# Optimization experiments

Measured on AMD Instinct MI355X. Metric: run time of the kernel, lower is better.

The kernel has to match this reference:

```python
import jax, jax.numpy as jnp
import numpy as np

LAMDA = 1.0


def setup_inputs() -> dict:
    key = jax.random.key(0)
    k1, k2, k3, k4 = jax.random.split(key, 4)
    B, C, D = 16384, 1000, 512
    logits = jax.random.normal(k1, (B, C), dtype=jnp.float32)
    labels = jax.random.randint(k2, (B,), 0, C, dtype=jnp.int64)
    features = jax.random.normal(k3, (B, D), dtype=jnp.float32)
    global_protos = jax.random.normal(k4, (C, D), dtype=jnp.float32)
    return {"logits": logits, "labels": labels, "features": features,
            "global_protos": global_protos}


def reference(logits, labels, features, global_protos):
    # --- classification loss: mean cross-entropy ---
    logp = jax.nn.log_softmax(logits, axis=-1)                 # [B, C]
    ce_loss = -jnp.take_along_axis(logp, labels[:, None], axis=1).mean()
    ce_loss = jnp.where(jnp.isfinite(ce_loss), ce_loss, 0.0)

    # --- prototype alignment loss ---
    # Every label has a (finite) global prototype, so the per-sample dict
    # loop reduces to: gather proto by label, per-sample MSE, mean over B.
    gathered = global_protos[labels]                           # [B, D]
    per_sample_mse = jnp.mean((features - gathered) ** 2, axis=-1)  # [B]
    proto_loss = per_sample_mse.mean()

    total_loss = ce_loss + LAMDA * proto_loss
    total_loss = jnp.where(jnp.isfinite(total_loss), total_loss, ce_loss)
    return (total_loss, ce_loss, proto_loss)
```

## Files before the change

### kernel.cpp

```cpp
#include <hip/hip_runtime.h>
#include <math.h>


#ifndef INFINITY
#define INFINITY __builtin_inff()
#endif

__global__ __launch_bounds__(256) void fedtgp_rows(
    const float* __restrict__ logits,
    const int*   __restrict__ labels,
    const float* __restrict__ features,
    const float* __restrict__ protos,
    double2* __restrict__ part,
    int B, int C, int D)
{
    const int tid  = threadIdx.x;
    const int lane = tid & 63;
    const int wv   = tid >> 6;
    const int row  = blockIdx.x * 4 + wv;
    const bool valid = (row < B);

    double2 res;
    res.x = 0.0; res.y = 0.0;

    if (valid) {
        const int    lab  = labels[row];
        const float* lrow = logits + (size_t)row * C;
        const float4* l4  = (const float4*)lrow;
        const int C4 = C >> 2;
        const int D4 = D >> 2;

        float4 v[4];
        #pragma unroll
        for (int k = 0; k < 4; ++k) {
            const int idx = lane + 64 * k;
            v[k] = (idx < C4) ? l4[idx]
                              : make_float4(-INFINITY, -INFINITY, -INFINITY, -INFINITY);
        }
        const float4* f4 = (const float4*)(features + (size_t)row * D);
        const float4* p4 = (const float4*)(protos   + (size_t)lab * D);
        float4 f0 = make_float4(0.f,0.f,0.f,0.f), p0 = f0, f1 = f0, p1 = f0;
        if (lane < D4)      { f0 = f4[lane];      p0 = p4[lane]; }
        if (lane + 64 < D4) { f1 = f4[lane + 64]; p1 = p4[lane + 64]; }
        const float ll = lrow[lab];

        float s = 0.f;
        #pragma unroll
        for (int k = 0; k < 4; ++k) {
            s += __expf(v[k].x) + __expf(v[k].y)
               + __expf(v[k].z) + __expf(v[k].w);
        }
        for (int idx = 256 + lane; idx < C4; idx += 64) {
            const float4 w = l4[idx];
            s += __expf(w.x) + __expf(w.y) + __expf(w.z) + __expf(w.w);
        }
        for (int c = (C4 << 2) + lane; c < C; c += 64)
            s += __expf(lrow[c]);

        float q;
        {
            const float ax = f0.x - p0.x, ay = f0.y - p0.y;
            const float az = f0.z - p0.z, aw = f0.w - p0.w;
            const float bx = f1.x - p1.x, by = f1.y - p1.y;
            const float bz = f1.z - p1.z, bw = f1.w - p1.w;
            q = ax*ax + ay*ay + az*az + aw*aw
              + bx*bx + by*by + bz*bz + bw*bw;
        }
        for (int idx = lane + 128; idx < D4; idx += 64) {
            const float4 f = f4[idx];
            const float4 p = p4[idx];
            const float dx = f.x - p.x, dy = f.y - p.y;
            const float dz = f.z - p.z, dw = f.w - p.w;
            q += dx*dx + dy*dy + dz*dz + dw*dw;
        }
        for (int d = (D4 << 2) + lane; d < D; d += 64)
        {
            const float df = features[(size_t)row * D + d]
                           - protos[(size_t)lab * D + d];
            q += df * df;
        }

        #pragma unroll
        for (int off = 32; off > 0; off >>= 1) {
            s += __shfl_xor(s, off, 64);
            q += __shfl_xor(q, off, 64);
        }

        res.x = (double)(__logf(s) - ll);
        res.y = (double)(q / (float)D);
    }

    if (lane == 0)
        part[blockIdx.x * 4 + wv] = res;
}

__global__ __launch_bounds__(1024) void fedtgp_finalize(
    const double2* __restrict__ part,
    float* __restrict__ out,
    int npart, double invB)
{
    const int tid  = threadIdx.x;
    const int lane = tid & 63;
    const int wv   = tid >> 6;
    __shared__ double rc[16];
    __shared__ double rp[16];

    double c = 0.0, p = 0.0;
    for (int i = tid; i < npart; i += 1024) {
        const double2 v = part[i];
        c += v.x;
        p += v.y;
    }
    #pragma unroll
    for (int off = 32; off > 0; off >>= 1) {
        c += __shfl_xor(c, off, 64);
        p += __shfl_xor(p, off, 64);
    }
    if (lane == 0) { rc[wv] = c; rp[wv] = p; }
    __syncthreads();

    if (tid == 0) {
        double cs = 0.0, ps = 0.0;
        #pragma unroll
        for (int k = 0; k < 16; ++k) { cs += rc[k]; ps += rp[k]; }
        float ce = (float)(cs * invB);
        float pl = (float)(ps * invB);
        if (!isfinite(ce)) ce = 0.0f;
        float tot = ce + pl;
        if (!isfinite(tot)) tot = ce;
        out[0] = tot;
        out[1] = ce;
        out[2] = pl;
    }
}

extern "C" void kernel_launch(void* const* d_in, const int* in_sizes, int n_in,
                              void* d_out, int out_size, void* d_ws, size_t ws_size,
                              hipStream_t stream)
{
    const float* logits   = (const float*)d_in[0];
    const int*   labels   = (const int*)  d_in[1];
    const float* features = (const float*)d_in[2];
    const float* protos   = (const float*)d_in[3];
    float* out = (float*)d_out;

    const int B = in_sizes[1];
    const int C = in_sizes[0] / B;
    const int D = in_sizes[2] / B;

    int nb = (B + 3) / 4;
    const size_t need = (size_t)nb * 4 * sizeof(double2);
    if (need > ws_size) {
        nb = (int)(ws_size / (4 * sizeof(double2)));
        if (nb < 1) nb = 1;
    }
    const int npart = nb * 4;

    double2* part = (double2*)d_ws;

    fedtgp_rows<<<nb, 256, 0, stream>>>(logits, labels, features, protos,
                                        part, B, C, D);
    fedtgp_finalize<<<1, 1024, 0, stream>>>(part, out, npart, 1.0 / (double)B);
}
```

Measured before the change: 125.8 us.

## Fuse finalize into row kernel via last-block atomic reduction and nontemporal loads

Merges the separate finalize kernel into the main row kernel. Each block reduces its four rows in shared memory, writes one partial pair with atomics, and the last block to increment a counter sums all partials and writes the outputs. Logits and features are read with nontemporal loads to reduce cache pollution. This removes a kernel launch and shrinks the partial array, but adds a memset of the counter header, atomics and a threadfence in every block.

```diff
diff --git a/kernel.cpp b/kernel.cpp
--- a/kernel.cpp
+++ b/kernel.cpp
@@ -6,13 +6,26 @@
 #define INFINITY __builtin_inff()
 #endif
 
-__global__ __launch_bounds__(256) void fedtgp_rows(
+typedef float fx4 __attribute__((ext_vector_type(4)));
+
+struct Header {
+    unsigned int cnt;
+    unsigned int pad[15];
+};
+
+__device__ __forceinline__ fx4 nt_load4(const float* p) {
+    return __builtin_nontemporal_load((const fx4*)p);
+}
+
+__global__ __launch_bounds__(256) void fedtgp_fused2(
     const float* __restrict__ logits,
     const int*   __restrict__ labels,
     const float* __restrict__ features,
     const float* __restrict__ protos,
-    double2* __restrict__ part,
-    int B, int C, int D)
+    Header* __restrict__ hdr,
+    unsigned long long* __restrict__ part,
+    float* __restrict__ out,
+    int B, int C, int D, double invB)
 {
     const int tid  = threadIdx.x;
     const int lane = tid & 63;
@@ -20,28 +33,30 @@
     const int row  = blockIdx.x * 4 + wv;
     const bool valid = (row < B);
 
-    double2 res;
-    res.x = 0.0; res.y = 0.0;
+    __shared__ double sc[4], sp[4];
+
+    double ce_w = 0.0, pl_w = 0.0;
 
     if (valid) {
         const int    lab  = labels[row];
         const float* lrow = logits + (size_t)row * C;
-        const float4* l4  = (const float4*)lrow;
         const int C4 = C >> 2;
         const int D4 = D >> 2;
 
-        float4 v[4];
+        fx4 v[4];
         #pragma unroll
         for (int k = 0; k < 4; ++k) {
             const int idx = lane + 64 * k;
-            v[k] = (idx < C4) ? l4[idx]
-                              : make_float4(-INFINITY, -INFINITY, -INFINITY, -INFINITY);
+            if (idx < C4) v[k] = nt_load4(lrow + 4 * idx);
+            else          v[k] = (fx4){-INFINITY, -INFINITY, -INFINITY, -INFINITY};
         }
-        const float4* f4 = (const float4*)(features + (size_t)row * D);
-        const float4* p4 = (const float4*)(protos   + (size_t)lab * D);
-        float4 f0 = make_float4(0.f,0.f,0.f,0.f), p0 = f0, f1 = f0, p1 = f0;
-        if (lane < D4)      { f0 = f4[lane];      p0 = p4[lane]; }
-        if (lane + 64 < D4) { f1 = f4[lane + 64]; p1 = p4[lane + 64]; }
+        const float* frow = features + (size_t)row * D;
+        const float* prow = protos   + (size_t)lab * D;
+        fx4 f0 = (fx4){0.f,0.f,0.f,0.f}, p0 = f0, f1 = f0, p1 = f0;
+        if (lane < D4)      { f0 = nt_load4(frow + 4 * lane);
+                              p0 = *(const fx4*)(prow + 4 * lane); }
+        if (lane + 64 < D4) { f1 = nt_load4(frow + 4 * (lane + 64));
+                              p1 = *(const fx4*)(prow + 4 * (lane + 64)); }
         const float ll = lrow[lab];
 
         float s = 0.f;
@@ -51,7 +66,7 @@
                + __expf(v[k].z) + __expf(v[k].w);
         }
         for (int idx = 256 + lane; idx < C4; idx += 64) {
-            const float4 w = l4[idx];
+            const fx4 w = *(const fx4*)(lrow + 4 * idx);
             s += __expf(w.x) + __expf(w.y) + __expf(w.z) + __expf(w.w);
         }
         for (int c = (C4 << 2) + lane; c < C; c += 64)
@@ -67,16 +82,14 @@
               + bx*bx + by*by + bz*bz + bw*bw;
         }
         for (int idx = lane + 128; idx < D4; idx += 64) {
-            const float4 f = f4[idx];
-            const float4 p = p4[idx];
+            const fx4 f = *(const fx4*)(frow + 4 * idx);
+            const fx4 p = *(const fx4*)(prow + 4 * idx);
             const float dx = f.x - p.x, dy = f.y - p.y;
             const float dz = f.z - p.z, dw = f.w - p.w;
             q += dx*dx + dy*dy + dz*dz + dw*dw;
         }
-        for (int d = (D4 << 2) + lane; d < D; d += 64)
-        {
-            const float df = features[(size_t)row * D + d]
-                           - protos[(size_t)lab * D + d];
+        for (int d = (D4 << 2) + lane; d < D; d += 64) {
+            const float df = frow[d] - prow[d];
             q += df * df;
         }
 
@@ -86,51 +99,58 @@
             q += __shfl_xor(q, off, 64);
         }
 
-        res.x = (double)(__logf(s) - ll);
-        res.y = (double)(q / (float)D);
+        ce_w = (double)(__logf(s) - ll);
+        pl_w = (double)(q / (float)D);
     }
 
-    if (lane == 0)
-        part[blockIdx.x * 4 + wv] = res;
-}
-
-__global__ __launch_bounds__(1024) void fedtgp_finalize(
-    const double2* __restrict__ part,
-    float* __restrict__ out,
-    int npart, double invB)
-{
-    const int tid  = threadIdx.x;
-    const int lane = tid & 63;
-    const int wv   = tid >> 6;
-    __shared__ double rc[16];
-    __shared__ double rp[16];
-
-    double c = 0.0, p = 0.0;
-    for (int i = tid; i < npart; i += 1024) {
-        const double2 v = part[i];
-        c += v.x;
-        p += v.y;
-    }
-    #pragma unroll
-    for (int off = 32; off > 0; off >>= 1) {
-        c += __shfl_xor(c, off, 64);
-        p += __shfl_xor(p, off, 64);
-    }
-    if (lane == 0) { rc[wv] = c; rp[wv] = p; }
+    if (lane == 0) { sc[wv] = ce_w; sp[wv] = pl_w; }
     __syncthreads();
 
     if (tid == 0) {
-        double cs = 0.0, ps = 0.0;
+        const double ce_b = sc[0] + sc[1] + sc[2] + sc[3];
+        const double pl_b = sp[0] + sp[1] + sp[2] + sp[3];
+        atomicExch(&part[(size_t)blockIdx.x * 2 + 0], __double_as_longlong(ce_b));
+        atomicExch(&part[(size_t)blockIdx.x * 2 + 1], __double_as_longlong(pl_b));
+        __threadfence();
+    }
+    __syncthreads();
+
+    __shared__ bool amLast;
+    if (tid == 0) {
+        const unsigned prev = atomicAdd(&hdr->cnt, 1u);
+        amLast = (prev == (unsigned)(gridDim.x - 1));
+    }
+    __syncthreads();
+
+    if (amLast) {
+        const int n2 = (int)gridDim.x;
+        double c = 0.0, p = 0.0;
+        for (int i = tid; i < n2; i += 256) {
+            const unsigned long long cb = atomicAdd(&part[(size_t)i * 2 + 0], 0ull);
+            const unsigned long long pb = atomicAdd(&part[(size_t)i * 2 + 1], 0ull);
+            c += __longlong_as_double(cb);
+            p += __longlong_as_double(pb);
+        }
         #pragma unroll
-        for (int k = 0; k < 16; ++k) { cs += rc[k]; ps += rp[k]; }
-        float ce = (float)(cs * invB);
-        float pl = (float)(ps * invB);
-        if (!isfinite(ce)) ce = 0.0f;
-        float tot = ce + pl;
-        if (!isfinite(tot)) tot = ce;
-        out[0] = tot;
-        out[1] = ce;
-        out[2] = pl;
+        for (int off = 32; off > 0; off >>= 1) {
+            c += __shfl_xor(c, off, 64);
+            p += __shfl_xor(p, off, 64);
+        }
+        __shared__ double rc[4], rp[4];
+        if (lane == 0) { rc[wv] = c; rp[wv] = p; }
+        __syncthreads();
+        if (tid == 0) {
+            const double cs = rc[0] + rc[1] + rc[2] + rc[3];
+            const double ps = rp[0] + rp[1] + rp[2] + rp[3];
+            float ce = (float)(cs * invB);
+            float pl = (float)(ps * invB);
+            if (!isfinite(ce)) ce = 0.0f;
+            float tot = ce + pl;
+            if (!isfinite(tot)) tot = ce;
+            out[0] = tot;
+            out[1] = ce;
+            out[2] = pl;
+        }
     }
 }
 
@@ -149,16 +169,18 @@
     const int D = in_sizes[2] / B;
 
     int nb = (B + 3) / 4;
-    const size_t need = (size_t)nb * 4 * sizeof(double2);
+    const size_t need = sizeof(Header) + (size_t)nb * 2 * sizeof(unsigned long long);
     if (need > ws_size) {
-        nb = (int)(ws_size / (4 * sizeof(double2)));
+        nb = (int)((ws_size - sizeof(Header)) / (2 * sizeof(unsigned long long)));
         if (nb < 1) nb = 1;
     }
-    const int npart = nb * 4;
 
-    double2* part = (double2*)d_ws;
+    Header* hdr = (Header*)d_ws;
+    unsigned long long* part = (unsigned long long*)((char*)d_ws + sizeof(Header));
 
-    fedtgp_rows<<<nb, 256, 0, stream>>>(logits, labels, features, protos,
-                                        part, B, C, D);
-    fedtgp_finalize<<<1, 1024, 0, stream>>>(part, out, npart, 1.0 / (double)B);
+    (void)hipMemsetAsync(d_ws, 0, sizeof(Header), stream);
+
+    fedtgp_fused2<<<nb, 256, 0, stream>>>(logits, labels, features, protos,
+                                          hdr, part, out, B, C, D,
+                                          1.0 / (double)B);
 }
```

New measurement: 309.9 us. 146% more time.

## Process four rows per wave with double-buffered prefetch and nontemporal loads

Applied to the files above, without the earlier changes.

Each wave now handles four consecutive rows instead of one, issuing the loads for the next row before reducing the current one so memory latency overlaps with the exp and MSE work. Logits and features are read with nontemporal loads to avoid polluting cache, while prototypes still use normal loads because rows are reused across samples. The grid shrinks by a factor of four, giving fewer waves in flight and more registers per thread, which can cut the parallelism available to hide latency.

```diff
diff --git a/kernel.cpp b/kernel.cpp
--- a/kernel.cpp
+++ b/kernel.cpp
@@ -5,6 +5,31 @@
 #ifndef INFINITY
 #define INFINITY __builtin_inff()
 #endif
+
+typedef float fx4 __attribute__((ext_vector_type(4)));
+
+__device__ __forceinline__ fx4 nt_load4(const float* p) {
+    return __builtin_nontemporal_load((const fx4*)p);
+}
+
+__device__ __forceinline__ void load_row(
+    const float* __restrict__ lrow, const float* __restrict__ frow,
+    const float* __restrict__ prow, int lane, int C4, int D4, int lab,
+    fx4 v[4], fx4& f0, fx4& f1, fx4& p0, fx4& p1, float& ll)
+{
+    #pragma unroll
+    for (int k = 0; k < 4; ++k) {
+        const int idx = lane + 64 * k;
+        if (idx < C4) v[k] = nt_load4(lrow + 4 * idx);
+        else          v[k] = (fx4){-INFINITY, -INFINITY, -INFINITY, -INFINITY};
+    }
+    f0 = p0 = f1 = p1 = (fx4){0.f, 0.f, 0.f, 0.f};
+    if (lane < D4)      { f0 = nt_load4(frow + 4 * lane);
+                          p0 = *(const fx4*)(prow + 4 * lane); }
+    if (lane + 64 < D4) { f1 = nt_load4(frow + 4 * (lane + 64));
+                          p1 = *(const fx4*)(prow + 4 * (lane + 64)); }
+    ll = lrow[lab];
+}
 
 __global__ __launch_bounds__(256) void fedtgp_rows(
     const float* __restrict__ logits,
@@ -17,81 +42,104 @@
     const int tid  = threadIdx.x;
     const int lane = tid & 63;
     const int wv   = tid >> 6;
-    const int row  = blockIdx.x * 4 + wv;
-    const bool valid = (row < B);
-
-    double2 res;
-    res.x = 0.0; res.y = 0.0;
-
-    if (valid) {
-        const int    lab  = labels[row];
-        const float* lrow = logits + (size_t)row * C;
-        const float4* l4  = (const float4*)lrow;
-        const int C4 = C >> 2;
-        const int D4 = D >> 2;
-
-        float4 v[4];
-        #pragma unroll
-        for (int k = 0; k < 4; ++k) {
-            const int idx = lane + 64 * k;
-            v[k] = (idx < C4) ? l4[idx]
-                              : make_float4(-INFINITY, -INFINITY, -INFINITY, -INFINITY);
+    const int wave = blockIdx.x * 4 + wv;
+    const int base_row = wave * 4;
+
+    const int C4 = C >> 2;
+    const int D4 = D >> 2;
+
+    fx4 v[2][4], f0[2], f1[2], p0[2], p1[2];
+    float ll[2];
+    const float* lrow[2];
+    const float* frow[2];
+    const float* prow[2];
+    bool ok[2];
+
+    double ce_acc = 0.0, pl_acc = 0.0;
+
+    {
+        const int row = base_row;
+        ok[0] = (row < B);
+        if (ok[0]) {
+            const int lab = labels[row];
+            lrow[0] = logits   + (size_t)row * C;
+            frow[0] = features + (size_t)row * D;
+            prow[0] = protos   + (size_t)lab * D;
+            load_row(lrow[0], frow[0], prow[0], lane, C4, D4, lab,
+                     v[0], f0[0], f1[0], p0[0], p1[0], ll[0]);
         }
-        const float4* f4 = (const float4*)(features + (size_t)row * D);
-        const float4* p4 = (const float4*)(protos   + (size_t)lab * D);
-        float4 f0 = make_float4(0.f,0.f,0.f,0.f), p0 = f0, f1 = f0, p1 = f0;
-        if (lane < D4)      { f0 = f4[lane];      p0 = p4[lane]; }
-        if (lane + 64 < D4) { f1 = f4[lane + 64]; p1 = p4[lane + 64]; }
-        const float ll = lrow[lab];
-
-        float s = 0.f;
-        #pragma unroll
-        for (int k = 0; k < 4; ++k) {
-            s += __expf(v[k].x) + __expf(v[k].y)
-               + __expf(v[k].z) + __expf(v[k].w);
+    }
+
+    #pragma unroll
+    for (int r = 0; r < 4; ++r) {
+        const int cur = r & 1;
+        const int nxt = cur ^ 1;
+
+        if (r + 1 < 4) {
+            const int row = base_row + r + 1;
+            ok[nxt] = (row < B);
+            if (ok[nxt]) {
+                const int lab = labels[row];
+                lrow[nxt] = logits   + (size_t)row * C;
+                frow[nxt] = features + (size_t)row * D;
+                prow[nxt] = protos   + (size_t)lab * D;
+                load_row(lrow[nxt], frow[nxt], prow[nxt], lane, C4, D4, lab,
+                         v[nxt], f0[nxt], f1[nxt], p0[nxt], p1[nxt], ll[nxt]);
+            }
         }
-        for (int idx = 256 + lane; idx < C4; idx += 64) {
-            const float4 w = l4[idx];
-            s += __expf(w.x) + __expf(w.y) + __expf(w.z) + __expf(w.w);
+
+        if (ok[cur]) {
+            float s = 0.f;
+            #pragma unroll
+            for (int k = 0; k < 4; ++k) {
+                s += __expf(v[cur][k].x) + __expf(v[cur][k].y)
+                   + __expf(v[cur][k].z) + __expf(v[cur][k].w);
+            }
+            for (int idx = 256 + lane; idx < C4; idx += 64) {
+                const fx4 w = *(const fx4*)(lrow[cur] + 4 * idx);
+                s += __expf(w.x) + __expf(w.y) + __expf(w.z) + __expf(w.w);
+            }
+            for (int c = (C4 << 2) + lane; c < C; c += 64)
+                s += __expf(lrow[cur][c]);
+
+            float q;
+            {
+                const float ax = f0[cur].x - p0[cur].x, ay = f0[cur].y - p0[cur].y;
+                const float az = f0[cur].z - p0[cur].z, aw = f0[cur].w - p0[cur].w;
+                const float bx = f1[cur].x - p1[cur].x, by = f1[cur].y - p1[cur].y;
+                const float bz = f1[cur].z - p1[cur].z, bw = f1[cur].w - p1[cur].w;
+                q = ax*ax + ay*ay + az*az + aw*aw
+                  + bx*bx + by*by + bz*bz + bw*bw;
+            }
+            for (int idx = lane + 128; idx < D4; idx += 64) {
+                const fx4 f = *(const fx4*)(frow[cur] + 4 * idx);
+                const fx4 p = *(const fx4*)(prow[cur] + 4 * idx);
+                const float dx = f.x - p.x, dy = f.y - p.y;
+                const float dz = f.z - p.z, dw = f.w - p.w;
+                q += dx*dx + dy*dy + dz*dz + dw*dw;
+            }
+            for (int d = (D4 << 2) + lane; d < D; d += 64) {
+                const float df = frow[cur][d] - prow[cur][d];
+                q += df * df;
+            }
+
+            #pragma unroll
+            for (int off = 32; off > 0; off >>= 1) {
+                s += __shfl_xor(s, off, 64);
+                q += __shfl_xor(q, off, 64);
+            }
+
+            if (lane == 0) {
+                ce_acc += (double)(__logf(s) - ll[cur]);
+                pl_acc += (double)(q / (float)D);
+            }
         }
-        for (int c = (C4 << 2) + lane; c < C; c += 64)
-            s += __expf(lrow[c]);
-
-        float q;
-        {
-            const float ax = f0.x - p0.x, ay = f0.y - p0.y;
-            const float az = f0.z - p0.z, aw = f0.w - p0.w;
-            const float bx = f1.x - p1.x, by = f1.y - p1.y;
-            const float bz = f1.z - p1.z, bw = f1.w - p1.w;
-            q = ax*ax + ay*ay + az*az + aw*aw
-              + bx*bx + by*by + bz*bz + bw*bw;
-        }
-        for (int idx = lane + 128; idx < D4; idx += 64) {
-            const float4 f = f4[idx];
-            const float4 p = p4[idx];
-            const float dx = f.x - p.x, dy = f.y - p.y;
-            const float dz = f.z - p.z, dw = f.w - p.w;
-            q += dx*dx + dy*dy + dz*dz + dw*dw;
-        }
-        for (int d = (D4 << 2) + lane; d < D; d += 64)
-        {
-            const float df = features[(size_t)row * D + d]
-                           - protos[(size_t)lab * D + d];
-            q += df * df;
-        }
-
-        #pragma unroll
-        for (int off = 32; off > 0; off >>= 1) {
-            s += __shfl_xor(s, off, 64);
-            q += __shfl_xor(q, off, 64);
-        }
-
-        res.x = (double)(__logf(s) - ll);
-        res.y = (double)(q / (float)D);
-    }
-
-    if (lane == 0)
-        part[blockIdx.x * 4 + wv] = res;
+    }
+
+    if (lane == 0) {
+        double2 res; res.x = ce_acc; res.y = pl_acc;
+        part[wave] = res;
+    }
 }
 
 __global__ __launch_bounds__(1024) void fedtgp_finalize(
@@ -148,7 +196,7 @@
     const int C = in_sizes[0] / B;
     const int D = in_sizes[2] / B;
 
-    int nb = (B + 3) / 4;
+    int nb = (B + 15) / 16;
     const size_t need = (size_t)nb * 4 * sizeof(double2);
     if (need > ws_size) {
         nb = (int)(ws_size / (4 * sizeof(double2)));
```

Result: slower. 129.0 us (+2.6%).
